# Kernel tuning notes

Hardware: AMD Instinct MI355X
Metric: run time of the kernel (lower is better)

The kernel has to match this reference:

```python
import jax, jax.numpy as jnp
import numpy as np

NUM_LAYERS = 4   # i: conv layers in Unary
K_DISP = 128     # k: disparity labels
FEAT_C = 64      # unary feature channels


def _conv3x3(x, w, b):
    # x: [B,C,H,W], w: [O,I,3,3] (OIHW), padding SAME, stride 1
    y = jax.lax.conv_general_dilated(
        x, w, window_strides=(1, 1), padding='SAME',
        dimension_numbers=('NCHW', 'OIHW', 'NCHW'))
    return y + b[None, :, None, None]


def _unary(x, Ws, bs):
    # i conv layers, tanh between layers, linear output (siamese unary net)
    n = len(Ws)
    for i in range(n):
        x = _conv3x3(x, Ws[i], bs[i])
        if i < n - 1:
            x = jnp.tanh(x)
    return x


def _correlation(phiL, phiR, k):
    # corr[b,d,y,x] = sum_c phiL[b,c,y,x] * phiR[b,c,y,x-d], zero out-of-range
    B, C, H, W = phiL.shape
    Rpad = jnp.pad(phiR, ((0, 0), (0, 0), (0, 0), (k - 1, 0)))  # zero-pad left

    def step(_, d):
        # shifted right feature map: Rpad[..., k-1-d : k-1-d+W] == phiR shifted right by d
        Rs = jax.lax.dynamic_slice_in_dim(Rpad, k - 1 - d, W, axis=3)
        return None, jnp.einsum('bchw,bchw->bhw', phiL, Rs)

    _, ys = jax.lax.scan(step, None, jnp.arange(k))  # [k,B,H,W]
    return jnp.moveaxis(ys, 0, 1)                    # [B,k,H,W]


def setup_inputs() -> dict:
    key = jax.random.key(0)
    ks = jax.random.split(key, 2 + NUM_LAYERS)
    B, H, W = 2, 384, 1280
    d = {
        'l': jax.random.normal(ks[0], (B, 3, H, W), jnp.float32),
        'r': jax.random.normal(ks[1], (B, 3, H, W), jnp.float32),
    }
    chans = [3] + [FEAT_C] * NUM_LAYERS

    def xavier(k_, shape):
        fan_in = shape[1] * shape[2] * shape[3]
        fan_out = shape[0] * shape[2] * shape[3]
        std = float(np.sqrt(2.0 / (fan_in + fan_out)))
        return jax.random.normal(k_, shape, jnp.float32) * std

    for i in range(NUM_LAYERS):
        d[f'W{i}'] = xavier(ks[2 + i], (chans[i + 1], chans[i], 3, 3))
        d[f'b{i}'] = jnp.zeros((chans[i + 1],), jnp.float32)
    return d


def reference(l, r, W0, b0, W1, b1, W2, b2, W3, b3):
    Ws = [W0, W1, W2, W3]
    bs = [b0, b1, b2, b3]
    phi_left = _unary(l, Ws, bs)
    phi_right = _unary(r, Ws, bs)
    return _correlation(phi_left, phi_right, K_DISP)  # [B, k, H, W]
```

## Files before the change

kernel.cpp:

```cpp
#include <hip/hip_runtime.h>

#define HH 384
#define WW 1280

typedef unsigned short u16;
typedef unsigned int u32;
typedef __attribute__((ext_vector_type(8))) short short8;
typedef __attribute__((ext_vector_type(8))) unsigned short u16x8;
typedef __attribute__((ext_vector_type(4))) float f32x4;

__device__ __forceinline__ float bf2f(u16 u){ union{u32 i;float f;}v; v.i=((u32)u)<<16; return v.f; }
__device__ __forceinline__ u16 f2bf(float f){ union{float f;u32 i;}v; v.f=f; u32 r=v.i+0x7fffu+((v.i>>16)&1u); return (u16)(r>>16); }
__device__ __forceinline__ float ftanh(float x){
  float e = __expf(2.0f*x);
  return 1.0f - 2.0f/(e+1.0f);
}
__device__ __forceinline__ void gload_lds16(const void* g, void* l){
  __builtin_amdgcn_global_load_lds((const __attribute__((address_space(1))) void*)g,
                                   (__attribute__((address_space(3))) void*)l, 16, 0, 0);
}

__global__ __launch_bounds__(256) void prep_weights(const float* __restrict__ W1,
    const float* __restrict__ W2, const float* __restrict__ W3, u16* __restrict__ wf){
  int idx = blockIdx.x*256 + threadIdx.x;
  if (idx >= 110592) return;
  int m    = idx & 63;
  int oc   = (idx>>6) & 63;
  int tap  = (idx>>12) % 9;
  int layer= idx / 36864;
  int ic   = m ^ ((oc&7)<<3);
  const float* Ws = layer==0 ? W1 : (layer==1 ? W2 : W3);
  wf[idx] = f2bf(Ws[(oc*64+ic)*9 + tap]);
}

__global__ __launch_bounds__(256) void conv0_kernel(const float* __restrict__ img,
    const float* __restrict__ W0, const float* __restrict__ b0, u16* __restrict__ out){
  int x = blockIdx.x*256 + threadIdx.x;
  int y = blockIdx.y;
  int n = blockIdx.z;
  const float* in = img + (size_t)n*3*HH*WW;
  float acc[64];
  #pragma unroll
  for (int o=0;o<64;++o) acc[o] = b0[o];
  #pragma unroll
  for (int ic=0; ic<3; ++ic)
  #pragma unroll
  for (int dy=0; dy<3; ++dy){
    int gy = y + dy - 1;
    #pragma unroll
    for (int dx=0; dx<3; ++dx){
      int gx = x + dx - 1;
      float v = 0.f;
      if (gy>=0 && gy<HH && (unsigned)gx < (unsigned)WW)
        v = in[((size_t)ic*HH + gy)*WW + gx];
      #pragma unroll
      for (int o=0;o<64;++o)
        acc[o] = fmaf(v, W0[(o*3+ic)*9 + dy*3 + dx], acc[o]);
    }
  }
  u16* op = out + ((size_t)((n*HH + y)*WW) + x)*64;
  #pragma unroll
  for (int cc=0; cc<8; ++cc){
    u16x8 v;
    #pragma unroll
    for (int k=0;k<8;++k) v[k] = f2bf(ftanh(acc[cc*8+k]));
    *(u16x8*)(op + cc*8) = v;
  }
}

template<bool TANH>
__global__ __launch_bounds__(256) void conv64_kernel(const u16* __restrict__ in,
    const u16* __restrict__ wfL, const float* __restrict__ bias,
    const u16* __restrict__ zpad, u16* __restrict__ out){
  __shared__ __align__(16) u16 tile[6*66*64];
  __shared__ __align__(16) u16 wbuf[3][4096];
  const int tid = threadIdx.x;
  int id = blockIdx.x;
  id = (id & 7)*480 + (id >> 3);
  const int x0 = (id % 20)*64;
  const int y0 = ((id / 20) % 96)*4;
  const int n  = id / 1920;
  const u16* inN = in + (size_t)n*HH*WW*64;

  for (int q0 = 0; q0 < 3168; q0 += 256){
    int q = q0 + tid;
    if (q < 3168){
      int row = q / 528;
      int rem = q - row*528;
      int col = rem >> 3;
      int j   = rem & 7;
      int gy = y0 - 1 + row;
      int gx = x0 - 1 + col;
      const u16* g;
      if ((unsigned)gy < (unsigned)HH && (unsigned)gx < (unsigned)WW)
        g = inN + (((size_t)(gy*WW + gx))<<6) + ((j ^ (col&7))<<3);
      else
        g = zpad + (j<<3);
      gload_lds16(g, &tile[(size_t)(q & ~63)*8]);
    }
  }
  #pragma unroll
  for (int t=0; t<2; ++t)
    #pragma unroll
    for (int c=0; c<2; ++c){
      int q = c*256 + tid;
      gload_lds16(wfL + (size_t)t*4096 + (size_t)q*8, &wbuf[t][(q & ~63)*8]);
    }
  asm volatile("s_waitcnt vmcnt(2)" ::: "memory");
  __builtin_amdgcn_s_barrier();
  __builtin_amdgcn_sched_barrier(0);

  const int lane = tid & 63;
  const int wv = tid >> 6;
  const int l15 = lane & 15;
  const int lh  = lane >> 4;

  f32x4 acc[4][4];
  #pragma unroll
  for (int mt=0;mt<4;++mt)
    #pragma unroll
    for (int nt=0;nt<4;++nt) acc[mt][nt] = (f32x4){0.f,0.f,0.f,0.f};

  #pragma unroll
  for (int tap = 0; tap < 9; ++tap){
    const int dy = tap/3, dx = tap%3;
    if (tap <= 6){
      const u16* wsrc = wfL + (size_t)(tap+2)*4096;
      u16* wdst = wbuf[(tap+2)%3];
      #pragma unroll
      for (int c=0;c<2;++c){
        int q = c*256 + tid;
        gload_lds16(wsrc + (size_t)q*8, &wdst[(q & ~63)*8]);
      }
    }
    const char* wb = (const char*)wbuf[tap%3];
    const char* tb = (const char*)tile;
    const int xorA = ((l15 + dx)&7)<<4;
    const int xorB = (l15&7)<<4;
    #pragma unroll
    for (int kh=0; kh<2; ++kh){
      const int kbyte = kh*64 + lh*16;
      short8 a[4], b[4];
      #pragma unroll
      for (int mt=0; mt<4; ++mt){
        int col = mt*16 + l15 + dx;
        a[mt] = *(const short8*)(tb + ((wv+dy)*66 + col)*128 + (kbyte ^ xorA));
      }
      #pragma unroll
      for (int nt=0; nt<4; ++nt){
        int oc = nt*16 + l15;
        b[nt] = *(const short8*)(wb + oc*128 + (kbyte ^ xorB));
      }
      #pragma unroll
      for (int mt=0; mt<4; ++mt)
        #pragma unroll
        for (int nt=0; nt<4; ++nt)
          acc[mt][nt] = __builtin_amdgcn_mfma_f32_16x16x32_bf16(a[mt], b[nt], acc[mt][nt], 0,0,0);
    }
    if (tap < 8){
      if (tap <= 6) asm volatile("s_waitcnt vmcnt(2)" ::: "memory");
      else          asm volatile("s_waitcnt vmcnt(0)" ::: "memory");
      __builtin_amdgcn_s_barrier();
      __builtin_amdgcn_sched_barrier(0);
    }
  }

  float bv[4];
  #pragma unroll
  for (int nt=0;nt<4;++nt) bv[nt] = bias[nt*16 + l15];
  const int gy = y0 + wv;
  u16* outR = out + (size_t)n*HH*WW*64 + (size_t)gy*WW*64;
  #pragma unroll
  for (int mt=0; mt<4; ++mt){
    #pragma unroll
    for (int r=0; r<4; ++r){
      int x = x0 + mt*16 + lh*4 + r;
      u16* op = outR + (size_t)x*64 + l15;
      #pragma unroll
      for (int nt=0; nt<4; ++nt){
        float v = acc[mt][nt][r] + bv[nt];
        if (TANH) v = ftanh(v);
        op[nt*16] = f2bf(v);
      }
    }
  }
}

__global__ __launch_bounds__(256) void corr_kernel(const u16* __restrict__ phiL,
    const u16* __restrict__ phiR, float* __restrict__ out){
  __shared__ __align__(16) float band[128*65];
  const int tid = threadIdx.x;
  int id = blockIdx.x;
  id = (id & 7)*1920 + (id >> 3);
  const int x0 = (id % 20)*64;
  const int y  = (id / 20) % 384;
  const int b  = id / 7680;
  const u16* Lrow = phiL + ((size_t)(b*HH + y)*WW)*64;
  const u16* Rrow = phiR + ((size_t)(b*HH + y)*WW)*64;

  const int lane = tid & 63;
  const int wv   = tid >> 6;
  const int l15  = lane & 15;
  const int lh   = lane >> 4;

  f32x4 acc[4][3];
  #pragma unroll
  for (int mt=0;mt<4;++mt)
    #pragma unroll
    for (int nt=0;nt<3;++nt) acc[mt][nt] = (f32x4){0.f,0.f,0.f,0.f};

  #pragma unroll
  for (int kh=0; kh<2; ++kh){
    const int koff = kh*32 + lh*8;
    short8 a[4], bb[3];
    #pragma unroll
    for (int mt=0; mt<4; ++mt)
      a[mt] = *(const short8*)(Lrow + (size_t)(x0 + mt*16 + l15)*64 + koff);
    #pragma unroll
    for (int nt=0; nt<3; ++nt){
      int gx = x0 - 128 + wv*48 + nt*16 + l15;
      short8 z = (short8){0,0,0,0,0,0,0,0};
      bb[nt] = (gx >= 0) ? *(const short8*)(Rrow + (size_t)gx*64 + koff) : z;
    }
    #pragma unroll
    for (int mt=0; mt<4; ++mt)
      #pragma unroll
      for (int nt=0; nt<3; ++nt)
        acc[mt][nt] = __builtin_amdgcn_mfma_f32_16x16x32_bf16(a[mt], bb[nt], acc[mt][nt], 0,0,0);
  }

  #pragma unroll
  for (int mt=0; mt<4; ++mt){
    #pragma unroll
    for (int nt=0; nt<3; ++nt){
      int jr = wv*48 + nt*16 + l15;
      #pragma unroll
      for (int r=0; r<4; ++r){
        int x = mt*16 + lh*4 + r;
        int d = x - jr + 128;
        if ((unsigned)d < 128u) band[d*65 + x] = acc[mt][nt][r];
      }
    }
  }
  __syncthreads();

  float* ob = out + ((size_t)(b*128)*HH + (size_t)y)*WW + x0;
  #pragma unroll
  for (int it=0; it<8; ++it){
    int c = it*256 + tid;
    int d = c>>4, xq = c&15;
    const float* bp = &band[d*65 + xq*4];
    float4 v = make_float4(bp[0], bp[1], bp[2], bp[3]);
    *(float4*)&ob[(size_t)d*HH*WW + xq*4] = v;
  }
}

extern "C" void kernel_launch(void* const* d_in, const int* in_sizes, int n_in,
                              void* d_out, int out_size, void* d_ws, size_t ws_size,
                              hipStream_t stream){
  const float* l  = (const float*)d_in[0];
  const float* r  = (const float*)d_in[1];
  const float* W0 = (const float*)d_in[2];
  const float* b0 = (const float*)d_in[3];
  const float* W1 = (const float*)d_in[4];
  const float* b1 = (const float*)d_in[5];
  const float* W2 = (const float*)d_in[6];
  const float* b2 = (const float*)d_in[7];
  const float* W3 = (const float*)d_in[8];
  const float* b3 = (const float*)d_in[9];
  float* out = (float*)d_out;

  const size_t SIDE = (size_t)2*HH*WW*64;
  u16* wf   = (u16*)d_ws;
  u16* zpad = (u16*)((char*)d_ws + (1u<<20));
  u16* BL   = (u16*)((char*)d_ws + (2u<<20));
  u16* BR   = BL + SIDE;
  u16* A    = (u16*)d_out;

  hipMemsetAsync(zpad, 0, 256, stream);
  prep_weights<<<dim3(432), dim3(256), 0, stream>>>(W1, W2, W3, wf);

  for (int s = 0; s < 2; ++s){
    const float* img = s ? r : l;
    u16* B = s ? BR : BL;
    conv0_kernel<<<dim3(WW/256, HH, 2), dim3(256), 0, stream>>>(img, W0, b0, A);
    conv64_kernel<true ><<<dim3(3840), dim3(256), 0, stream>>>(A, wf + 0*36864, b1, zpad, B);
    conv64_kernel<true ><<<dim3(3840), dim3(256), 0, stream>>>(B, wf + 1*36864, b2, zpad, A);
    conv64_kernel<false><<<dim3(3840), dim3(256), 0, stream>>>(A, wf + 2*36864, b3, zpad, B);
  }

  corr_kernel<<<dim3(15360), dim3(256), 0, stream>>>(BL, BR, out);
}
```

Before: 1.044 ms.

## Split conv64 input tile into channel halves and pipeline 18 half-tap steps

Restructures the 3x3 conv64 kernel so the input tile is staged as two 32-channel halves, with weights reorganized per (tap, half) into 4-deep rotating LDS buffers. Compute starts once the first channel half arrives, while the second half and later weight slices stream in. Halo columns are now loaded through registers instead of per-element zero-pad redirects, and the XCD-aware block remapping is replaced by a plain 3D grid. The finer-grained steps double the number of barriers and may hurt L2 locality.

```diff
diff --git a/kernel.cpp b/kernel.cpp
--- a/kernel.cpp
+++ b/kernel.cpp
@@ -21,16 +21,18 @@
 }
 
 __global__ __launch_bounds__(256) void prep_weights(const float* __restrict__ W1,
-    const float* __restrict__ W2, const float* __restrict__ W3, u16* __restrict__ wf){
+    const float* __restrict__ W2, const float* __restrict__ W3, u16* __restrict__ wq){
   int idx = blockIdx.x*256 + threadIdx.x;
   if (idx >= 110592) return;
-  int m    = idx & 63;
-  int oc   = (idx>>6) & 63;
+  int mp   = idx & 31;
+  int oc   = (idx>>5) & 63;
+  int kh   = (idx>>11) & 1;
   int tap  = (idx>>12) % 9;
   int layer= idx / 36864;
-  int ic   = m ^ ((oc&7)<<3);
+  int m    = mp ^ (((oc>>1)&3)<<3);
+  int ic   = kh*32 + m;
   const float* Ws = layer==0 ? W1 : (layer==1 ? W2 : W3);
-  wf[idx] = f2bf(Ws[(oc*64+ic)*9 + tap]);
+  wq[idx] = f2bf(Ws[(oc*64+ic)*9 + tap]);
 }
 
 __global__ __launch_bounds__(256) void conv0_kernel(const float* __restrict__ img,
@@ -72,48 +74,72 @@
 __global__ __launch_bounds__(256) void conv64_kernel(const u16* __restrict__ in,
     const u16* __restrict__ wfL, const float* __restrict__ bias,
     const u16* __restrict__ zpad, u16* __restrict__ out){
-  __shared__ __align__(16) u16 tile[6*66*64];
-  __shared__ __align__(16) u16 wbuf[3][4096];
+  __shared__ __align__(16) u16 tileH[2][12672];
+  __shared__ __align__(16) u16 wbuf[4*2048];
   const int tid = threadIdx.x;
-  int id = blockIdx.x;
-  id = (id & 7)*480 + (id >> 3);
-  const int x0 = (id % 20)*64;
-  const int y0 = ((id / 20) % 96)*4;
-  const int n  = id / 1920;
+  const int x0 = blockIdx.x*64;
+  const int y0 = blockIdx.y*4;
+  const int n  = blockIdx.z;
   const u16* inN = in + (size_t)n*HH*WW*64;
 
-  for (int q0 = 0; q0 < 3168; q0 += 256){
-    int q = q0 + tid;
-    if (q < 3168){
-      int row = q / 528;
-      int rem = q - row*528;
-      int col = rem >> 3;
-      int j   = rem & 7;
-      int gy = y0 - 1 + row;
-      int gx = x0 - 1 + col;
-      const u16* g;
-      if ((unsigned)gy < (unsigned)HH && (unsigned)gx < (unsigned)WW)
-        g = inN + (((size_t)(gy*WW + gx))<<6) + ((j ^ (col&7))<<3);
-      else
-        g = zpad + (j<<3);
-      gload_lds16(g, &tile[(size_t)(q & ~63)*8]);
-    }
-  }
-  #pragma unroll
-  for (int t=0; t<2; ++t)
-    #pragma unroll
-    for (int c=0; c<2; ++c){
-      int q = c*256 + tid;
-      gload_lds16(wfL + (size_t)t*4096 + (size_t)q*8, &wbuf[t][(q & ~63)*8]);
-    }
-  asm volatile("s_waitcnt vmcnt(2)" ::: "memory");
-  __builtin_amdgcn_s_barrier();
-  __builtin_amdgcn_sched_barrier(0);
-
   const int lane = tid & 63;
-  const int wv = tid >> 6;
+  const int wv  = tid >> 6;
   const int l15 = lane & 15;
   const int lh  = lane >> 4;
+  const int bswz = (lh*16) ^ (((l15>>1)&3)<<4);
+
+#define PREFW(kk) gload_lds16( \
+    wfL + (size_t)(((((kk)%9)*2 + ((kk)/9))*2048) + tid*8), \
+    &wbuf[((kk)&3)*2048 + (tid & ~63)*8])
+
+#define STAGE_TILE(h) \
+  _Pragma("unroll") \
+  for (int k6 = 0; k6 < 6; ++k6){ \
+    int p  = k6*256 + tid; \
+    int r  = p >> 8, c64 = (p >> 2) & 63, j2 = p & 3; \
+    int cc_ = c64 + 1; \
+    int gy = y0 - 1 + r; \
+    const u16* g = ((unsigned)gy < (unsigned)HH) \
+      ? inN + (((size_t)(gy*WW + x0 + c64))<<6) + (h)*32 + ((j2 ^ ((cc_>>1)&3))<<3) \
+      : zpad + (j2<<3); \
+    int p0 = p & ~63; \
+    int r0 = p0 >> 8, c0 = (p0 >> 2) & 63; \
+    gload_lds16(g, &tileH[h][(r0*66 + c0 + 1)*32]); \
+  }
+
+  const u16* hsrc = zpad;
+  int hdst = -1;
+  {
+    int i = tid;
+    if (i < 96){
+      int h    = i / 48;
+      int i48  = i % 48;
+      int r    = i48 >> 3;
+      int side = (i48 >> 2) & 1;
+      int jj   = i48 & 3;
+      int col  = side ? 65 : 0;
+      int gy   = y0 - 1 + r;
+      int gx   = side ? x0 + 64 : x0 - 1;
+      if ((unsigned)gy < (unsigned)HH && (unsigned)gx < (unsigned)WW)
+        hsrc = inN + (((size_t)(gy*WW + gx))<<6) + h*32 + jj*8;
+      hdst = h*12672 + (r*66 + col)*32 + jj*8;
+    }
+  }
+  u16x8 haloV = *(const u16x8*)hsrc;
+  __builtin_amdgcn_sched_barrier(0);
+  PREFW(0);
+  __builtin_amdgcn_sched_barrier(0);
+  STAGE_TILE(0)
+  __builtin_amdgcn_sched_barrier(0);
+  PREFW(1); PREFW(2); PREFW(3);
+  __builtin_amdgcn_sched_barrier(0);
+  STAGE_TILE(1)
+  __builtin_amdgcn_sched_barrier(0);
+  asm volatile("s_waitcnt vmcnt(9)" ::: "memory");
+  if (hdst >= 0) *(u16x8*)&tileH[0][hdst] = haloV;
+  asm volatile("s_waitcnt lgkmcnt(0)" ::: "memory");
+  __builtin_amdgcn_s_barrier();
+  __builtin_amdgcn_sched_barrier(0);
 
   f32x4 acc[4][4];
   #pragma unroll
@@ -121,49 +147,53 @@
     #pragma unroll
     for (int nt=0;nt<4;++nt) acc[mt][nt] = (f32x4){0.f,0.f,0.f,0.f};
 
-  #pragma unroll
-  for (int tap = 0; tap < 9; ++tap){
-    const int dy = tap/3, dx = tap%3;
-    if (tap <= 6){
-      const u16* wsrc = wfL + (size_t)(tap+2)*4096;
-      u16* wdst = wbuf[(tap+2)%3];
-      #pragma unroll
-      for (int c=0;c<2;++c){
-        int q = c*256 + tid;
-        gload_lds16(wsrc + (size_t)q*8, &wdst[(q & ~63)*8]);
-      }
-    }
-    const char* wb = (const char*)wbuf[tap%3];
-    const char* tb = (const char*)tile;
-    const int xorA = ((l15 + dx)&7)<<4;
-    const int xorB = (l15&7)<<4;
-    #pragma unroll
-    for (int kh=0; kh<2; ++kh){
-      const int kbyte = kh*64 + lh*16;
-      short8 a[4], b[4];
-      #pragma unroll
-      for (int mt=0; mt<4; ++mt){
-        int col = mt*16 + l15 + dx;
-        a[mt] = *(const short8*)(tb + ((wv+dy)*66 + col)*128 + (kbyte ^ xorA));
-      }
-      #pragma unroll
-      for (int nt=0; nt<4; ++nt){
-        int oc = nt*16 + l15;
-        b[nt] = *(const short8*)(wb + oc*128 + (kbyte ^ xorB));
-      }
-      #pragma unroll
-      for (int mt=0; mt<4; ++mt)
-        #pragma unroll
-        for (int nt=0; nt<4; ++nt)
-          acc[mt][nt] = __builtin_amdgcn_mfma_f32_16x16x32_bf16(a[mt], b[nt], acc[mt][nt], 0,0,0);
-    }
-    if (tap < 8){
-      if (tap <= 6) asm volatile("s_waitcnt vmcnt(2)" ::: "memory");
-      else          asm volatile("s_waitcnt vmcnt(0)" ::: "memory");
-      __builtin_amdgcn_s_barrier();
-      __builtin_amdgcn_sched_barrier(0);
-    }
-  }
+#define TAPK(k) { \
+    const int tap_ = (k)%9, h_ = (k)/9, dy_ = tap_/3, dx_ = tap_%3; \
+    if ((k) >= 1 && (k) <= 14){ PREFW((k)+3); } \
+    const char* th_ = (const char*)&tileH[h_][0]; \
+    const char* wb_ = (const char*)&wbuf[((k)&3)*2048]; \
+    short8 a_[4], b_[4]; \
+    _Pragma("unroll") \
+    for (int mt=0; mt<4; ++mt){ \
+      int c_ = mt*16 + l15 + dx_; \
+      a_[mt] = *(const short8*)(th_ + ((wv+dy_)*66 + c_)*64 + ((lh*16) ^ (((c_>>1)&3)<<4))); \
+    } \
+    _Pragma("unroll") \
+    for (int nt=0; nt<4; ++nt) \
+      b_[nt] = *(const short8*)(wb_ + (nt*16+l15)*64 + bswz); \
+    _Pragma("unroll") \
+    for (int mt=0; mt<4; ++mt) \
+      _Pragma("unroll") \
+      for (int nt=0; nt<4; ++nt) \
+        acc[mt][nt] = __builtin_amdgcn_mfma_f32_16x16x32_bf16(a_[mt], b_[nt], acc[mt][nt], 0,0,0); \
+  }
+#define BARR(VMLIT) \
+    asm volatile("s_waitcnt vmcnt(" #VMLIT ")" ::: "memory"); \
+    __builtin_amdgcn_s_barrier(); \
+    __builtin_amdgcn_sched_barrier(0);
+
+  TAPK(0)  BARR(8)
+  TAPK(1)  BARR(8)
+  TAPK(2)  BARR(8)
+  TAPK(3)  BARR(2)
+  TAPK(4)  BARR(2)
+  TAPK(5)  BARR(2)
+  TAPK(6)  BARR(2)
+  TAPK(7)  BARR(2)
+  TAPK(8)  BARR(2)
+  TAPK(9)  BARR(2)
+  TAPK(10) BARR(2)
+  TAPK(11) BARR(2)
+  TAPK(12) BARR(2)
+  TAPK(13) BARR(2)
+  TAPK(14) BARR(2)
+  TAPK(15) BARR(1)
+  TAPK(16) BARR(0)
+  TAPK(17)
+#undef TAPK
+#undef BARR
+#undef PREFW
+#undef STAGE_TILE
 
   float bv[4];
   #pragma unroll
@@ -284,9 +314,9 @@
     const float* img = s ? r : l;
     u16* B = s ? BR : BL;
     conv0_kernel<<<dim3(WW/256, HH, 2), dim3(256), 0, stream>>>(img, W0, b0, A);
-    conv64_kernel<true ><<<dim3(3840), dim3(256), 0, stream>>>(A, wf + 0*36864, b1, zpad, B);
-    conv64_kernel<true ><<<dim3(3840), dim3(256), 0, stream>>>(B, wf + 1*36864, b2, zpad, A);
-    conv64_kernel<false><<<dim3(3840), dim3(256), 0, stream>>>(A, wf + 2*36864, b3, zpad, B);
+    conv64_kernel<true ><<<dim3(WW/64, HH/4, 2), dim3(256), 0, stream>>>(A, wf + 0*36864, b1, zpad, B);
+    conv64_kernel<true ><<<dim3(WW/64, HH/4, 2), dim3(256), 0, stream>>>(B, wf + 1*36864, b2, zpad, A);
+    conv64_kernel<false><<<dim3(WW/64, HH/4, 2), dim3(256), 0, stream>>>(A, wf + 2*36864, b3, zpad, B);
   }
 
   corr_kernel<<<dim3(15360), dim3(256), 0, stream>>>(BL, BR, out);
```

New measurement: 1.151 ms. +10.2%, slower.
